# Performance work log

Measured on AMD Instinct MI355X. Metric: run time of the kernel, lower is better.

The kernel has to match this reference:

```python
import jax, jax.numpy as jnp
import numpy as np

B, C_IN, C_OUT, H, W = 16, 256, 256, 64, 64
RANK, ORDER = 16, 2
EPS = 1e-5


def setup_inputs() -> dict:
    key = jax.random.key(0)
    k1, k2, k3 = jax.random.split(key, 3)
    x = jax.random.normal(k1, (B, C_IN, H, W), dtype=jnp.float32)
    # torch init: w_core ~ N(0, 1/(C_in*rank)), w_out ~ N(0, 1/rank)
    w_core = jax.random.normal(k2, (RANK, C_IN, RANK), dtype=jnp.float32) * (1.0 / (C_IN * RANK))
    w_out = jax.random.normal(k3, (RANK, C_OUT, RANK), dtype=jnp.float32) * (1.0 / RANK)
    return {"x": x, "w_core": w_core, "w_out": w_out}


def reference(x, w_core, w_out):
    # Per-pixel tensor-ring 1x1 conv.
    # Original chain for order=2 (share_core):
    #   T = einsum('achw,rck->arhwk', x, w_core)
    #   out = einsum('aebcf,afbcg,gdh->aedbch', T, T, w_out)
    #   y   = einsum('arohwr->aohw', out)   # ring trace over e==h
    # Equivalent: M[a,h,w] is rank x rank; P = M^order; y_d = tr(P @ W_d)
    M = jnp.einsum('achw,rck->ahwrk', x, w_core)  # [B,H,W,r,r]
    P = M
    for _ in range(ORDER - 1):
        P = jnp.einsum('ahwef,ahwfg->ahweg', P, M)
    y = jnp.einsum('ahweg,gde->adhw', P, w_out)  # [B,C_out,H,W]
    # InstanceNorm2d (affine=False, biased variance) + Softsign
    mean = jnp.mean(y, axis=(2, 3), keepdims=True)
    var = jnp.var(y, axis=(2, 3), keepdims=True)
    yn = (y - mean) * jax.lax.rsqrt(var + EPS)
    return yn / (1.0 + jnp.abs(yn))
```

## Files before the change

kernel.cpp:

```cpp
#include <hip/hip_runtime.h>

#define HW 4096
#define NC 256
#define ND 256

typedef _Float16 half4_t __attribute__((ext_vector_type(4)));
typedef _Float16 half8_t __attribute__((ext_vector_type(8)));
typedef float floatx2 __attribute__((ext_vector_type(2)));
typedef float floatx4 __attribute__((ext_vector_type(4)));

#define MSCALE 64.0f
#define INV_MSCALE2 (1.0f / 4096.0f)

__global__ __launch_bounds__(256) void prep_weights(
        const float* __restrict__ w_core, const float* __restrict__ w_out,
        _Float16* __restrict__ W1p, _Float16* __restrict__ W2p) {
    int tid = blockIdx.x * 256 + threadIdx.x;
    int l   = tid & 63;
    int rt  = (tid >> 6) & 15;
    int ks  = (tid >> 10) & 7;
    int sel = tid >> 13;
    int row = l & 15, kg = l >> 4;
    half8_t v;
    if (sel == 0) {
        int r = rt, k = row;
#pragma unroll
        for (int j = 0; j < 8; ++j) {
            int c = ks * 32 + kg * 8 + j;
            v[j] = (_Float16)(w_core[r * 4096 + c * 16 + k] * MSCALE);
        }
        *(half8_t*)&W1p[(size_t)((ks * 16 + rt) * 64 + l) * 8] = v;
    } else {
        int d = rt * 16 + row;
#pragma unroll
        for (int j = 0; j < 8; ++j) {
            int eg = ks * 32 + kg * 8 + j, e = eg >> 4, g = eg & 15;
            v[j] = (_Float16)w_out[g * 4096 + d * 16 + e];
        }
        *(half8_t*)&W2p[(size_t)((ks * 16 + rt) * 64 + l) * 8] = v;
    }
}

__global__ __launch_bounds__(256, 2) void compute_y(
        const float* __restrict__ x, const _Float16* __restrict__ W1p,
        const _Float16* __restrict__ W2p, float* __restrict__ y,
        float* __restrict__ ssum, float* __restrict__ ssq) {
    __shared__ __align__(16) _Float16 R1[16384];
    __shared__ __align__(16) _Float16 R2[16384];

    const int t = threadIdx.x;
    const int l = t & 63, w = t >> 6;
    const int a = blockIdx.x >> 6;
    const int pixbase = (blockIdx.x & 63) * 64;
    const int row16 = l & 15, kg = l >> 4;
    const float* xa = x + (size_t)a * NC * HW + pixbase;

    {
        const int cl  = t >> 4;
        const int pxq = (t & 15) * 4;
#pragma unroll
        for (int q = 0; q < 16; ++q) {
            int c = q * 16 + cl;
            float4 v = *(const float4*)&xa[(size_t)c * HW + pxq];
            int cu = c >> 3, cr = c & 7;
            float vv[4] = {v.x, v.y, v.z, v.w};
#pragma unroll
            for (int i = 0; i < 4; ++i) {
                int px = pxq + i;
                R1[px * 256 + (cu ^ (px & 15)) * 8 + cr] = (_Float16)vv[i];
            }
        }
    }
    __syncthreads();

    floatx4 acc[4][4];
#pragma unroll
    for (int i = 0; i < 4; ++i)
#pragma unroll
        for (int j = 0; j < 4; ++j) acc[i][j] = (floatx4){0.f, 0.f, 0.f, 0.f};
    {
        const half8_t* W1v = (const half8_t*)W1p;
        for (int ks = 0; ks < 8; ++ks) {
            half8_t af[4];
#pragma unroll
            for (int rq = 0; rq < 4; ++rq)
                af[rq] = W1v[(ks * 16 + w * 4 + rq) * 64 + l];
#pragma unroll
            for (int pt = 0; pt < 4; ++pt) {
                const int px = pt * 16 + row16;
                half8_t bf = *(const half8_t*)
                    &R1[px * 256 + (((ks * 4 + kg) ^ row16) << 3)];
#pragma unroll
                for (int rq = 0; rq < 4; ++rq)
                    acc[rq][pt] = __builtin_amdgcn_mfma_f32_16x16x32_f16(
                                      af[rq], bf, acc[rq][pt], 0, 0, 0);
            }
        }
    }
#pragma unroll
    for (int rq = 0; rq < 4; ++rq) {
        const int rk4 = (w * 4 + rq) * 4 + kg;
#pragma unroll
        for (int pt = 0; pt < 4; ++pt) {
            const int px = pt * 16 + row16;
            half4_t hv;
#pragma unroll
            for (int r2 = 0; r2 < 4; ++r2) hv[r2] = (_Float16)acc[rq][pt][r2];
            *(half4_t*)&R2[px * 256 + ((rk4 ^ row16) << 2)] = hv;
        }
    }
    __syncthreads();

    {
        const int p = t >> 2, qe = t & 3, ps = p & 15;
        const _Float16* Mp = &R2[p * 256];
        float Af[4][16];
#pragma unroll
        for (int i = 0; i < 4; ++i) {
#pragma unroll
            for (int f4 = 0; f4 < 4; ++f4) {
                half4_t v = *(const half4_t*)
                    &Mp[((((qe * 4 + i) * 4 + f4) ^ ps) << 2)];
#pragma unroll
                for (int j = 0; j < 4; ++j) Af[i][f4 * 4 + j] = (float)v[j];
            }
        }
        floatx2 Pacc[4][8];
#pragma unroll
        for (int i = 0; i < 4; ++i)
#pragma unroll
            for (int g2 = 0; g2 < 8; ++g2) Pacc[i][g2] = (floatx2){0.f, 0.f};
#pragma unroll
        for (int f = 0; f < 16; ++f) {
            floatx2 Bg[8];
#pragma unroll
            for (int g4 = 0; g4 < 4; ++g4) {
                half4_t v = *(const half4_t*)
                    &Mp[(((f * 4 + g4) ^ ps) << 2)];
                Bg[g4 * 2]     = (floatx2){(float)v[0], (float)v[1]};
                Bg[g4 * 2 + 1] = (floatx2){(float)v[2], (float)v[3]};
            }
#pragma unroll
            for (int i = 0; i < 4; ++i) {
                floatx2 a2 = {Af[i][f], Af[i][f]};
#pragma unroll
                for (int g2 = 0; g2 < 8; ++g2)
                    Pacc[i][g2] = __builtin_elementwise_fma(a2, Bg[g2], Pacc[i][g2]);
            }
        }
#pragma unroll
        for (int i = 0; i < 4; ++i) {
            const int e = qe * 4 + i;
#pragma unroll
            for (int h2 = 0; h2 < 2; ++h2) {
                half8_t hv;
#pragma unroll
                for (int j = 0; j < 8; ++j)
                    hv[j] = (_Float16)Pacc[i][h2 * 4 + (j >> 1)][j & 1];
                *(half8_t*)&R1[p * 256 + (((e * 2 + h2) ^ ps) << 3)] = hv;
            }
        }
    }
    __syncthreads();

    floatx4 cacc[4][4];
#pragma unroll
    for (int i = 0; i < 4; ++i)
#pragma unroll
        for (int j = 0; j < 4; ++j) cacc[i][j] = (floatx4){0.f, 0.f, 0.f, 0.f};
    {
        const half8_t* W2v = (const half8_t*)W2p;
        for (int ks = 0; ks < 8; ++ks) {
            half8_t af[4];
#pragma unroll
            for (int dq = 0; dq < 4; ++dq)
                af[dq] = W2v[(ks * 16 + w * 4 + dq) * 64 + l];
#pragma unroll
            for (int pt = 0; pt < 4; ++pt) {
                const int px = pt * 16 + row16;
                half8_t bf = *(const half8_t*)
                    &R1[px * 256 + (((ks * 4 + kg) ^ row16) << 3)];
#pragma unroll
                for (int dq = 0; dq < 4; ++dq)
                    cacc[dq][pt] = __builtin_amdgcn_mfma_f32_16x16x32_f16(
                                       af[dq], bf, cacc[dq][pt], 0, 0, 0);
            }
        }
    }

    float* ya = y + (size_t)a * ND * HW + pixbase;
#pragma unroll
    for (int dq = 0; dq < 4; ++dq) {
        const int dbase = (w * 4 + dq) * 16 + kg * 4;
#pragma unroll
        for (int r2 = 0; r2 < 4; ++r2) {
            const int d = dbase + r2;
            float s = 0.f, q2 = 0.f;
#pragma unroll
            for (int pt = 0; pt < 4; ++pt) {
                float v = cacc[dq][pt][r2] * INV_MSCALE2;
                ya[(size_t)d * HW + pt * 16 + row16] = v;
                s += v; q2 += v * v;
            }
#pragma unroll
            for (int off = 1; off < 16; off <<= 1) {
                s  += __shfl_xor(s, off);
                q2 += __shfl_xor(q2, off);
            }
            if (row16 == 0) {
                atomicAdd(&ssum[a * 256 + d], s);
                atomicAdd(&ssq [a * 256 + d], q2);
            }
        }
    }
}

__global__ __launch_bounds__(256) void stats_finalize(
        const float* __restrict__ ssum, const float* __restrict__ ssq,
        float* __restrict__ mean_o, float* __restrict__ istd_o) {
    int i = blockIdx.x * 256 + threadIdx.x;
    float m = ssum[i] * (1.f / HW);
    float v = ssq[i] * (1.f / HW) - m * m;
    mean_o[i] = m;
    istd_o[i] = rsqrtf(v + 1e-5f);
}

__global__ __launch_bounds__(256) void finalize_kernel(
        float* __restrict__ y, const float* __restrict__ mean_a,
        const float* __restrict__ istd_a) {
    const int i4 = blockIdx.x * 256 + threadIdx.x;
    const int ad = i4 >> 10;
    const float m = mean_a[ad], s = istd_a[ad];
    float4 v = ((const float4*)y)[i4];
    float vv[4] = {v.x, v.y, v.z, v.w};
#pragma unroll
    for (int lq = 0; lq < 4; ++lq) {
        float z = (vv[lq] - m) * s;
        vv[lq] = z / (1.f + fabsf(z));
    }
    ((float4*)y)[i4] = make_float4(vv[0], vv[1], vv[2], vv[3]);
}

extern "C" void kernel_launch(void* const* d_in, const int* in_sizes, int n_in,
                              void* d_out, int out_size, void* d_ws, size_t ws_size,
                              hipStream_t stream) {
    const float* x      = (const float*)d_in[0];
    const float* w_core = (const float*)d_in[1];
    const float* w_out  = (const float*)d_in[2];
    float* y = (float*)d_out;

    _Float16* W1p = (_Float16*)d_ws;
    _Float16* W2p = W1p + 65536;
    float* ssum   = (float*)(W2p + 65536);
    float* ssq    = ssum + 4096;
    float* mean_a = ssq + 4096;
    float* istd_a = mean_a + 4096;

    hipMemsetAsync(ssum, 0, 2 * 4096 * sizeof(float), stream);
    prep_weights<<<64, 256, 0, stream>>>(w_core, w_out, W1p, W2p);
    compute_y<<<1024, 256, 0, stream>>>(x, W1p, W2p, y, ssum, ssq);
    stats_finalize<<<16, 256, 0, stream>>>(ssum, ssq, mean_a, istd_a);
    finalize_kernel<<<16384, 256, 0, stream>>>(y, mean_a, istd_a);
}
```

Baseline: 83.91 us.

## Store unnormalized y as fp16 in workspace and normalize into fp32 output

When the workspace is large enough, compute_y writes the pre-normalization result as unscaled fp16 to a workspace buffer instead of fp32 to the output. The finalize pass then reads half the bytes and writes fp32, with epsilon rescaled to match the unscaled values. The x-tile load is restructured so each thread gathers eight channels per pixel and does one 16-byte shared store, and the e index mapping in the M^2 step is permuted. It also adds an unused preload of pb fragments, which risks extra register pressure, and the fp16 intermediate adds rounding and possible overflow risk.

Result: slower. 86.32 us (+2.9%).

```diff
diff --git a/kernel.cpp b/kernel.cpp
--- a/kernel.cpp
+++ b/kernel.cpp
@@ -3,6 +3,7 @@
 #define HW 4096
 #define NC 256
 #define ND 256
+#define NB 16
 
 typedef _Float16 half4_t __attribute__((ext_vector_type(4)));
 typedef _Float16 half8_t __attribute__((ext_vector_type(8)));
@@ -11,6 +12,7 @@
 
 #define MSCALE 64.0f
 #define INV_MSCALE2 (1.0f / 4096.0f)
+#define EPS_SCALED (1e-5f * 4096.0f * 4096.0f)
 
 __global__ __launch_bounds__(256) void prep_weights(
         const float* __restrict__ w_core, const float* __restrict__ w_out,
@@ -41,10 +43,12 @@
     }
 }
 
+template<bool F16Y>
 __global__ __launch_bounds__(256, 2) void compute_y(
         const float* __restrict__ x, const _Float16* __restrict__ W1p,
         const _Float16* __restrict__ W2p, float* __restrict__ y,
-        float* __restrict__ ssum, float* __restrict__ ssq) {
+        _Float16* __restrict__ y16, float* __restrict__ ssum,
+        float* __restrict__ ssq) {
     __shared__ __align__(16) _Float16 R1[16384];
     __shared__ __align__(16) _Float16 R2[16384];
 
@@ -56,19 +60,16 @@
     const float* xa = x + (size_t)a * NC * HW + pixbase;
 
     {
-        const int cl  = t >> 4;
-        const int pxq = (t & 15) * 4;
-#pragma unroll
-        for (int q = 0; q < 16; ++q) {
-            int c = q * 16 + cl;
-            float4 v = *(const float4*)&xa[(size_t)c * HW + pxq];
-            int cu = c >> 3, cr = c & 7;
-            float vv[4] = {v.x, v.y, v.z, v.w};
-#pragma unroll
-            for (int i = 0; i < 4; ++i) {
-                int px = pxq + i;
-                R1[px * 256 + (cu ^ (px & 15)) * 8 + cr] = (_Float16)vv[i];
-            }
+        const int px = t & 63;
+        const int o0 = t >> 6;
+#pragma unroll
+        for (int q = 0; q < 8; ++q) {
+            const int oct = q * 4 + o0;
+            half8_t hv;
+#pragma unroll
+            for (int j = 0; j < 8; ++j)
+                hv[j] = (_Float16)xa[(size_t)(oct * 8 + j) * HW + px];
+            *(half8_t*)&R1[px * 256 + ((oct ^ (px & 15)) << 3)] = hv;
         }
     }
     __syncthreads();
@@ -117,10 +118,11 @@
         float Af[4][16];
 #pragma unroll
         for (int i = 0; i < 4; ++i) {
+            const int e = i * 4 + qe;
 #pragma unroll
             for (int f4 = 0; f4 < 4; ++f4) {
                 half4_t v = *(const half4_t*)
-                    &Mp[((((qe * 4 + i) * 4 + f4) ^ ps) << 2)];
+                    &Mp[(((e * 4 + f4) ^ ps) << 2)];
 #pragma unroll
                 for (int j = 0; j < 4; ++j) Af[i][f4 * 4 + j] = (float)v[j];
             }
@@ -150,7 +152,7 @@
         }
 #pragma unroll
         for (int i = 0; i < 4; ++i) {
-            const int e = qe * 4 + i;
+            const int e = i * 4 + qe;
 #pragma unroll
             for (int h2 = 0; h2 < 2; ++h2) {
                 half8_t hv;
@@ -162,6 +164,12 @@
         }
     }
     __syncthreads();
+
+    half8_t pb[8];
+#pragma unroll
+    for (int ks = 0; ks < 8; ++ks)
+        pb[ks] = *(const half8_t*)
+            &R1[(w * 16 + row16) * 256 + (((ks * 4 + kg) ^ row16) << 3)];
 
     floatx4 cacc[4][4];
 #pragma unroll
@@ -188,7 +196,8 @@
         }
     }
 
-    float* ya = y + (size_t)a * ND * HW + pixbase;
+    float*     ya   = y   + (size_t)a * ND * HW + pixbase;
+    _Float16*  ya16 = F16Y ? (y16 + (size_t)a * ND * HW + pixbase) : nullptr;
 #pragma unroll
     for (int dq = 0; dq < 4; ++dq) {
         const int dbase = (w * 4 + dq) * 16 + kg * 4;
@@ -198,8 +207,15 @@
             float s = 0.f, q2 = 0.f;
 #pragma unroll
             for (int pt = 0; pt < 4; ++pt) {
-                float v = cacc[dq][pt][r2] * INV_MSCALE2;
-                ya[(size_t)d * HW + pt * 16 + row16] = v;
+                float v;
+                if (F16Y) {
+                    _Float16 hv = (_Float16)cacc[dq][pt][r2];
+                    ya16[(size_t)d * HW + pt * 16 + row16] = hv;
+                    v = (float)hv;
+                } else {
+                    v = cacc[dq][pt][r2] * INV_MSCALE2;
+                    ya[(size_t)d * HW + pt * 16 + row16] = v;
+                }
                 s += v; q2 += v * v;
             }
 #pragma unroll
@@ -217,15 +233,37 @@
 
 __global__ __launch_bounds__(256) void stats_finalize(
         const float* __restrict__ ssum, const float* __restrict__ ssq,
-        float* __restrict__ mean_o, float* __restrict__ istd_o) {
+        float* __restrict__ mean_o, float* __restrict__ istd_o, float eps) {
     int i = blockIdx.x * 256 + threadIdx.x;
     float m = ssum[i] * (1.f / HW);
     float v = ssq[i] * (1.f / HW) - m * m;
     mean_o[i] = m;
-    istd_o[i] = rsqrtf(v + 1e-5f);
-}
-
-__global__ __launch_bounds__(256) void finalize_kernel(
+    istd_o[i] = rsqrtf(v + eps);
+}
+
+__global__ __launch_bounds__(256) void finalize_f16(
+        const _Float16* __restrict__ y16, const float* __restrict__ mean_a,
+        const float* __restrict__ istd_a, float* __restrict__ out) {
+    const size_t base = ((size_t)blockIdx.x * 256 + threadIdx.x) * 16;
+    const int ad = (int)(base >> 12);
+    const float m = mean_a[ad], s = istd_a[ad];
+    half8_t h0 = *(const half8_t*)&y16[base];
+    half8_t h1 = *(const half8_t*)&y16[base + 8];
+    float o[16];
+#pragma unroll
+    for (int j = 0; j < 8; ++j) {
+        float z0 = ((float)h0[j] - m) * s;
+        float z1 = ((float)h1[j] - m) * s;
+        o[j]     = z0 / (1.f + fabsf(z0));
+        o[8 + j] = z1 / (1.f + fabsf(z1));
+    }
+#pragma unroll
+    for (int q = 0; q < 4; ++q)
+        *(float4*)&out[base + q * 4] =
+            make_float4(o[q * 4], o[q * 4 + 1], o[q * 4 + 2], o[q * 4 + 3]);
+}
+
+__global__ __launch_bounds__(256) void finalize_f32(
         float* __restrict__ y, const float* __restrict__ mean_a,
         const float* __restrict__ istd_a) {
     const int i4 = blockIdx.x * 256 + threadIdx.x;
@@ -249,16 +287,27 @@
     const float* w_out  = (const float*)d_in[2];
     float* y = (float*)d_out;
 
-    _Float16* W1p = (_Float16*)d_ws;
-    _Float16* W2p = W1p + 65536;
-    float* ssum   = (float*)(W2p + 65536);
-    float* ssq    = ssum + 4096;
-    float* mean_a = ssq + 4096;
-    float* istd_a = mean_a + 4096;
+    char* wsb = (char*)d_ws;
+    _Float16* W1p = (_Float16*)wsb;
+    _Float16* W2p = (_Float16*)(wsb + 131072);
+    float* ssum   = (float*)(wsb + 262144);
+    float* ssq    = (float*)(wsb + 278528);
+    float* mean_a = (float*)(wsb + 294912);
+    float* istd_a = (float*)(wsb + 311296);
+    _Float16* y16 = (_Float16*)(wsb + 327680);
+
+    const size_t need_f16 = 327680 + (size_t)NB * ND * HW * sizeof(_Float16);
+    const bool use_f16 = ws_size >= need_f16;
 
     hipMemsetAsync(ssum, 0, 2 * 4096 * sizeof(float), stream);
     prep_weights<<<64, 256, 0, stream>>>(w_core, w_out, W1p, W2p);
-    compute_y<<<1024, 256, 0, stream>>>(x, W1p, W2p, y, ssum, ssq);
-    stats_finalize<<<16, 256, 0, stream>>>(ssum, ssq, mean_a, istd_a);
-    finalize_kernel<<<16384, 256, 0, stream>>>(y, mean_a, istd_a);
-}
+    if (use_f16) {
+        compute_y<true><<<1024, 256, 0, stream>>>(x, W1p, W2p, y, y16, ssum, ssq);
+        stats_finalize<<<16, 256, 0, stream>>>(ssum, ssq, mean_a, istd_a, EPS_SCALED);
+        finalize_f16<<<4096, 256, 0, stream>>>(y16, mean_a, istd_a, y);
+    } else {
+        compute_y<false><<<1024, 256, 0, stream>>>(x, W1p, W2p, y, nullptr, ssum, ssq);
+        stats_finalize<<<16, 256, 0, stream>>>(ssum, ssq, mean_a, istd_a, 1e-5f);
+        finalize_f32<<<16384, 256, 0, stream>>>(y, mean_a, istd_a);
+    }
+}
```
